# Kernel optimization log

Measured on AMD Instinct MI355X. Metric: run time of the kernel, lower is better.

Reference implementation:

```python
import jax, jax.numpy as jnp
import numpy as np

KAPPA = 0.5


def setup_inputs() -> dict:
    key = jax.random.key(0)
    embeddings = jax.random.normal(key, (8, 4096, 64), dtype=jnp.float32)
    return {"embeddings": embeddings}


def reference(embeddings):
    # logits[b, n, m] = kappa * <emb[b,n], emb[b,m]>   -> [B, N, N]
    logits = KAPPA * jnp.einsum("bnd,bmd->bnm", embeddings, embeddings)
    B = logits.shape[0]
    # logsumexp over both matrix dims, per batch element
    loss = jax.scipy.special.logsumexp(logits.reshape(B, -1), axis=1)
    return loss.mean()
```

## Files before the change

kernel.cpp:

```cpp
#include <hip/hip_runtime.h>
#include <math.h>

#define BATCH 8
#define NTOK  4096
#define DIM   64
#define BM    128
#define NT    (NTOK / BM)
#define TPB   (NT * (NT + 1) / 2)
#define KAPPA 0.5f
#define LOG2E 1.4426950408889634f
#define LN2   0.6931471805599453f

typedef _Float16 f16x8 __attribute__((ext_vector_type(8)));
typedef float    f32x16 __attribute__((ext_vector_type(16)));

__device__ __forceinline__ float EXP2(float x) {
#if __has_builtin(__builtin_amdgcn_exp2f)
    return __builtin_amdgcn_exp2f(x);
#else
    return __expf(x * LN2);
#endif
}

__global__ __launch_bounds__(256, 3)
void gram_lse_partial(const float* __restrict__ emb, float* __restrict__ ws) {
    __shared__ f16x8 As[8 * BM];
    __shared__ f16x8 Bs[8 * BM];

    const int tid = threadIdx.x;
    const int bb  = blockIdx.x;
    const int b   = bb / TPB;
    int t = bb - b * TPB;
    int ti = 0;
    while (t >= NT - ti) { t -= NT - ti; ++ti; }
    const int tj = ti + t;

    const float* embA = emb + ((size_t)b * NTOK + (size_t)ti * BM) * DIM;
    const float* embB = emb + ((size_t)b * NTOK + (size_t)tj * BM) * DIM;

    {
        const int g  = tid & 7;
        const int r0 = tid >> 3;
#pragma unroll
        for (int p = 0; p < 4; ++p) {
            const int row = r0 + 32 * p;
            const float4 a0 = *(const float4*)(embA + (size_t)row * DIM + g * 8);
            const float4 a1 = *(const float4*)(embA + (size_t)row * DIM + g * 8 + 4);
            const float4 b0 = *(const float4*)(embB + (size_t)row * DIM + g * 8);
            const float4 b1 = *(const float4*)(embB + (size_t)row * DIM + g * 8 + 4);
            f16x8 pa, pb;
            pa[0] = (_Float16)a0.x; pa[1] = (_Float16)a0.y;
            pa[2] = (_Float16)a0.z; pa[3] = (_Float16)a0.w;
            pa[4] = (_Float16)a1.x; pa[5] = (_Float16)a1.y;
            pa[6] = (_Float16)a1.z; pa[7] = (_Float16)a1.w;
            pb[0] = (_Float16)b0.x; pb[1] = (_Float16)b0.y;
            pb[2] = (_Float16)b0.z; pb[3] = (_Float16)b0.w;
            pb[4] = (_Float16)b1.x; pb[5] = (_Float16)b1.y;
            pb[6] = (_Float16)b1.z; pb[7] = (_Float16)b1.w;
            As[g * BM + (row ^ g)] = pa;
            Bs[g * BM + (row ^ g)] = pb;
        }
    }
    __syncthreads();

    const int lane = tid & 63;
    const int w    = tid >> 6;
    const int half = lane >> 5;
    const int ln31 = lane & 31;
    const int waveR = (w & 1) * 64;
    const int waveC = (w >> 1) * 64;

    f32x16 acc00 = {}, acc01 = {}, acc10 = {}, acc11 = {};
#pragma unroll
    for (int s = 0; s < 4; ++s) {
        const int g = 2 * s + half;
        const f16x8 a0 = As[g * BM + ((waveR + ln31) ^ g)];
        const f16x8 a1 = As[g * BM + ((waveR + 32 + ln31) ^ g)];
        const f16x8 b0 = Bs[g * BM + ((waveC + ln31) ^ g)];
        const f16x8 b1 = Bs[g * BM + ((waveC + 32 + ln31) ^ g)];
        acc00 = __builtin_amdgcn_mfma_f32_32x32x16_f16(a0, b0, acc00, 0, 0, 0);
        acc01 = __builtin_amdgcn_mfma_f32_32x32x16_f16(a0, b1, acc01, 0, 0, 0);
        acc10 = __builtin_amdgcn_mfma_f32_32x32x16_f16(a1, b0, acc10, 0, 0, 0);
        acc11 = __builtin_amdgcn_mfma_f32_32x32x16_f16(a1, b1, acc11, 0, 0, 0);
    }

    const float c2 = KAPPA * LOG2E;
    float lm = acc00[0];
#pragma unroll
    for (int e = 0; e < 16; ++e) {
        lm = fmaxf(lm, acc00[e]); lm = fmaxf(lm, acc01[e]);
        lm = fmaxf(lm, acc10[e]); lm = fmaxf(lm, acc11[e]);
    }
#pragma unroll
    for (int off = 32; off > 0; off >>= 1)
        lm = fmaxf(lm, __shfl_xor(lm, off));
    const float m2 = c2 * lm;

    float lsum = 0.f;
#pragma unroll
    for (int e = 0; e < 16; ++e) {
        lsum += EXP2(fmaf(c2, acc00[e], -m2));
        lsum += EXP2(fmaf(c2, acc01[e], -m2));
        lsum += EXP2(fmaf(c2, acc10[e], -m2));
        lsum += EXP2(fmaf(c2, acc11[e], -m2));
    }
#pragma unroll
    for (int off = 32; off > 0; off >>= 1)
        lsum += __shfl_xor(lsum, off);

    if (lane == 0) {
        const float wgt = (ti == tj) ? 1.f : 2.f;
        float2 pr; pr.x = m2; pr.y = wgt * lsum;
        *(float2*)(ws + ((size_t)bb * 4 + w) * 2) = pr;
    }
}

__global__ __launch_bounds__(512)
void reduce_lse(const float* __restrict__ ws, float* __restrict__ out) {
    const int tid  = threadIdx.x;
    const int w    = tid >> 6;
    const int lane = tid & 63;
    __shared__ float lse8[BATCH];

    const float* p = ws + (size_t)w * TPB * 8;
    float mv[33], lv[33];
#pragma unroll
    for (int c = 0; c < 33; ++c) {
        const float2 v = *(const float2*)(p + 2 * (lane + 64 * c));
        mv[c] = v.x; lv[c] = v.y;
    }
    float L = mv[0];
#pragma unroll
    for (int c = 1; c < 33; ++c) L = fmaxf(L, mv[c]);
#pragma unroll
    for (int off = 32; off > 0; off >>= 1) L = fmaxf(L, __shfl_xor(L, off));

    float s = 0.f;
#pragma unroll
    for (int c = 0; c < 33; ++c) s += lv[c] * EXP2(mv[c] - L);
#pragma unroll
    for (int off = 32; off > 0; off >>= 1) s += __shfl_xor(s, off);

    if (lane == 0) lse8[w] = LN2 * (L + log2f(s));
    __syncthreads();
    if (tid == 0) {
        float a = 0.f;
        for (int i = 0; i < BATCH; ++i) a += lse8[i];
        out[0] = a * (1.f / BATCH);
    }
}

extern "C" void kernel_launch(void* const* d_in, const int* in_sizes, int n_in,
                              void* d_out, int out_size, void* d_ws, size_t ws_size,
                              hipStream_t stream) {
    const float* emb = (const float*)d_in[0];
    float* out = (float*)d_out;
    float* ws  = (float*)d_ws;

    gram_lse_partial<<<BATCH * TPB, 256, 0, stream>>>(emb, ws);
    reduce_lse<<<1, 512, 0, stream>>>(ws, out);
}
```

Before: 80.49 us.

## Pre-convert embeddings to fp16 and stage tiles via direct global-to-LDS loads

Adds a separate conversion kernel that writes an fp16 copy of the embeddings to workspace once. The Gram-tile kernel then loads half-precision tiles straight into shared memory with global_load_lds, using a swizzled addressing scheme. This replaces the per-block fp32 loads and conversions, which were repeated for every tile pair. The cost is one extra kernel launch plus a workspace write and read, and the occupancy hint rises to 4 blocks.

```diff
diff --git a/kernel.cpp b/kernel.cpp
--- a/kernel.cpp
+++ b/kernel.cpp
@@ -22,49 +22,53 @@
 #endif
 }
 
-__global__ __launch_bounds__(256, 3)
-void gram_lse_partial(const float* __restrict__ emb, float* __restrict__ ws) {
-    __shared__ f16x8 As[8 * BM];
-    __shared__ f16x8 Bs[8 * BM];
+__global__ __launch_bounds__(256)
+void conv_f16(const float* __restrict__ emb, f16x8* __restrict__ o16) {
+    const size_t i = (size_t)blockIdx.x * 256 + threadIdx.x;
+    const float4 v0 = *(const float4*)(emb + i * 8);
+    const float4 v1 = *(const float4*)(emb + i * 8 + 4);
+    f16x8 p;
+    p[0] = (_Float16)v0.x; p[1] = (_Float16)v0.y;
+    p[2] = (_Float16)v0.z; p[3] = (_Float16)v0.w;
+    p[4] = (_Float16)v1.x; p[5] = (_Float16)v1.y;
+    p[6] = (_Float16)v1.z; p[7] = (_Float16)v1.w;
+    o16[i] = p;
+}
 
-    const int tid = threadIdx.x;
-    const int bb  = blockIdx.x;
-    const int b   = bb / TPB;
+__global__ __launch_bounds__(256, 4)
+void gram_lse_partial(const f16x8* __restrict__ w16, float* __restrict__ ws) {
+    __shared__ f16x8 S[2048];
+
+    const int tid  = threadIdx.x;
+    const int lane = tid & 63;
+    const int w    = tid >> 6;
+    const int bb   = blockIdx.x;
+    const int b    = bb / TPB;
     int t = bb - b * TPB;
     int ti = 0;
     while (t >= NT - ti) { t -= NT - ti; ++ti; }
     const int tj = ti + t;
 
-    const float* embA = emb + ((size_t)b * NTOK + (size_t)ti * BM) * DIM;
-    const float* embB = emb + ((size_t)b * NTOK + (size_t)tj * BM) * DIM;
+    const char* pA16 = (const char*)(w16 + ((size_t)b * NTOK + (size_t)ti * BM) * 8);
+    const char* pB16 = (const char*)(w16 + ((size_t)b * NTOK + (size_t)tj * BM) * 8);
 
     {
-        const int g  = tid & 7;
-        const int r0 = tid >> 3;
+        const char* pbase  = (w < 2) ? pA16 : pB16;
+        const int   upBase = (w & 1) * 512 + lane;
 #pragma unroll
-        for (int p = 0; p < 4; ++p) {
-            const int row = r0 + 32 * p;
-            const float4 a0 = *(const float4*)(embA + (size_t)row * DIM + g * 8);
-            const float4 a1 = *(const float4*)(embA + (size_t)row * DIM + g * 8 + 4);
-            const float4 b0 = *(const float4*)(embB + (size_t)row * DIM + g * 8);
-            const float4 b1 = *(const float4*)(embB + (size_t)row * DIM + g * 8 + 4);
-            f16x8 pa, pb;
-            pa[0] = (_Float16)a0.x; pa[1] = (_Float16)a0.y;
-            pa[2] = (_Float16)a0.z; pa[3] = (_Float16)a0.w;
-            pa[4] = (_Float16)a1.x; pa[5] = (_Float16)a1.y;
-            pa[6] = (_Float16)a1.z; pa[7] = (_Float16)a1.w;
-            pb[0] = (_Float16)b0.x; pb[1] = (_Float16)b0.y;
-            pb[2] = (_Float16)b0.z; pb[3] = (_Float16)b0.w;
-            pb[4] = (_Float16)b1.x; pb[5] = (_Float16)b1.y;
-            pb[6] = (_Float16)b1.z; pb[7] = (_Float16)b1.w;
-            As[g * BM + (row ^ g)] = pa;
-            Bs[g * BM + (row ^ g)] = pb;
+        for (int q = 0; q < 8; ++q) {
+            const int up  = upBase + q * 64;
+            const int g   = up >> 7;
+            const int rp  = up & 127;
+            const int off = (((rp ^ g) << 7) | (g << 4));
+            __builtin_amdgcn_global_load_lds(
+                (const __attribute__((address_space(1))) void*)(pbase + off),
+                (__attribute__((address_space(3))) void*)&S[(size_t)w * 512 + q * 64],
+                16, 0, 0);
         }
     }
     __syncthreads();
 
-    const int lane = tid & 63;
-    const int w    = tid >> 6;
     const int half = lane >> 5;
     const int ln31 = lane & 31;
     const int waveR = (w & 1) * 64;
@@ -74,10 +78,10 @@
 #pragma unroll
     for (int s = 0; s < 4; ++s) {
         const int g = 2 * s + half;
-        const f16x8 a0 = As[g * BM + ((waveR + ln31) ^ g)];
-        const f16x8 a1 = As[g * BM + ((waveR + 32 + ln31) ^ g)];
-        const f16x8 b0 = Bs[g * BM + ((waveC + ln31) ^ g)];
-        const f16x8 b1 = Bs[g * BM + ((waveC + 32 + ln31) ^ g)];
+        const f16x8 a0 = S[g * BM + ((waveR + ln31) ^ g)];
+        const f16x8 a1 = S[g * BM + ((waveR + 32 + ln31) ^ g)];
+        const f16x8 b0 = S[1024 + g * BM + ((waveC + ln31) ^ g)];
+        const f16x8 b1 = S[1024 + g * BM + ((waveC + 32 + ln31) ^ g)];
         acc00 = __builtin_amdgcn_mfma_f32_32x32x16_f16(a0, b0, acc00, 0, 0, 0);
         acc01 = __builtin_amdgcn_mfma_f32_32x32x16_f16(a0, b1, acc01, 0, 0, 0);
         acc10 = __builtin_amdgcn_mfma_f32_32x32x16_f16(a1, b0, acc10, 0, 0, 0);
@@ -155,8 +159,10 @@
                               hipStream_t stream) {
     const float* emb = (const float*)d_in[0];
     float* out = (float*)d_out;
-    float* ws  = (float*)d_ws;
+    f16x8* w16 = (f16x8*)d_ws;
+    float* prt = (float*)((char*)d_ws + (4u << 20));
 
-    gram_lse_partial<<<BATCH * TPB, 256, 0, stream>>>(emb, ws);
-    reduce_lse<<<1, 512, 0, stream>>>(ws, out);
+    conv_f16<<<NTOK * BATCH * DIM / 8 / 256, 256, 0, stream>>>(emb, w16);
+    gram_lse_partial<<<BATCH * TPB, 256, 0, stream>>>(w16, prt);
+    reduce_lse<<<1, 512, 0, stream>>>(prt, out);
 }
```

Measured after the change: 84.53 us. +5.0%, slower.
